# Performance work log

Hardware: AMD Instinct MI355X
Metric: run time of the kernel (lower is better)

## Reference

```python
import jax, jax.numpy as jnp
import numpy as np

B, C, HH, WW, HEADS = 4, 64, 256, 256, 8
CH = C // HEADS              # 8 per-head dim
HID = int(C * 2.66)          # 170
EPS_LN = 1e-5
EPS = 1e-6
QK_NORM = 1.0
# crpe windows for 8 heads: {3:2, 5:3, 7:3}; each conv input split = head_split*Ch*2
WINDOWS = [(3, 2), (5, 3), (7, 3)]


def conv2d(x, w, b=None, groups=1, pad=0):
    out = jax.lax.conv_general_dilated(
        x, w, (1, 1), [(pad, pad), (pad, pad)],
        dimension_numbers=('NCHW', 'OIHW', 'NCHW'), feature_group_count=groups)
    return out if b is None else out + b[None, :, None, None]


def setup_inputs() -> dict:
    key = jax.random.key(0)
    ks = jax.random.split(key, 32)
    p = lambda k, shp, s=0.05: jax.random.normal(k, shp, jnp.float32) * s
    inp = {
        'x': jax.random.normal(ks[0], (B, HH * WW, C), jnp.float32),
        'ln1_w': jnp.ones((C,), jnp.float32) + p(ks[1], (C,), 0.01),
        'sca_w': p(ks[2], (C, C, 1, 1)), 'sca_b': p(ks[3], (C,)),
        'dw1_w': p(ks[4], (2 * C, C, 1, 1)),          # 1x1 dim->2dim
        'dw2_w': p(ks[5], (C, 2, 3, 3)),              # grouped 3x3, groups=C, in/grp=2
        'qkv_w': p(ks[6], (3 * C, C, 1, 1)),
        'qkv_dw_w': p(ks[7], (3 * C, 1, 3, 3)),       # depthwise 3x3
        'temperature': jnp.ones((HEADS, 1, 1), jnp.float32),
        'r3_w': p(ks[8], (2, 2 * CH, 3, 3)), 'r3_b': p(ks[9], (2,)),
        'r5_w': p(ks[10], (3, 2 * CH, 5, 5)), 'r5_b': p(ks[11], (3,)),
        'r7_w': p(ks[12], (3, 2 * CH, 7, 7)), 'r7_b': p(ks[13], (3,)),
        'proj_w': p(ks[14], (C, C, 1, 1)),
        'ln2_w': jnp.ones((C,), jnp.float32) + p(ks[15], (C,), 0.01),
        'pin_w': p(ks[16], (2 * HID, C, 1, 1)),
        'ffn_dw_w': p(ks[17], (2 * HID, 1, 3, 3)),
        'pout_w': p(ks[18], (C, HID, 1, 1)),
        'H': HH, 'W': WW,
    }
    return inp


def biasfree_ln(x, w):
    # BiasFree LayerNorm over channel dim of NCHW (var only, no mean-subtract)
    sigma = jnp.var(x, axis=1, keepdims=True)
    return x / jnp.sqrt(sigma + EPS_LN) * w[None, :, None, None]


def refine_att(q, k, H, W, convs):
    # q: (B,h,N,Ch)  k: (B,h,Ch,N) -> per-head conv relative position map (B,h,N,1)
    b, h, N, Ch = q.shape
    q_img = q.transpose(0, 1, 3, 2).reshape(b, h, Ch, H, W)
    k_img = k.reshape(b, h, Ch, H, W)
    qk = jnp.concatenate([q_img, k_img], axis=2).reshape(b, h * 2 * Ch, H, W)
    splits = np.cumsum([s * 2 * Ch for _, s in WINDOWS])[:-1]
    parts = jnp.split(qk, splits, axis=1)
    outs = [conv2d(xp, wt, bs, groups=g, pad=win // 2)
            for (win, g), (wt, bs), xp in zip(WINDOWS, convs, parts)]
    att = jnp.concatenate(outs, axis=1)           # (b, h, H, W)
    return att.reshape(b, h, 1, H * W).transpose(0, 1, 3, 2)  # (b,h,N,1)


def attention(x, sca_w, sca_b, dw1_w, dw2_w, qkv_w, qkv_dw_w, temperature,
              refine_convs, proj_w, H, W):
    b, c, _, _ = x.shape
    N = H * W
    xsca = conv2d(jnp.mean(x, axis=(2, 3), keepdims=True), sca_w, sca_b)
    x1 = conv2d(conv2d(x, dw1_w), dw2_w, groups=c, pad=1)
    qkv = conv2d(conv2d(x, qkv_w), qkv_dw_w, groups=3 * c, pad=1)
    q, k, v = jnp.split(qkv, 3, axis=1)
    q = q.reshape(b, HEADS, CH, N).transpose(0, 1, 3, 2)  # b h N Ch
    k = k.reshape(b, HEADS, CH, N)                        # b h Ch N
    v = v.reshape(b, HEADS, CH, N).transpose(0, 1, 3, 2)  # b h N Ch
    q = q / (jnp.linalg.norm(q, axis=-1, keepdims=True) / QK_NORM + EPS)
    k = k / (jnp.linalg.norm(k, axis=-2, keepdims=True) / QK_NORM + EPS)
    refine_w = jax.nn.sigmoid(refine_att(q, k, H, W, refine_convs))
    attn = k @ v                                           # b h Ch Ch
    out_num = jnp.sum(v, axis=-2, keepdims=True) + q @ attn
    ksum = jnp.sum(k, axis=-1, keepdims=True)              # b h Ch 1
    out_den = jnp.asarray(N, q.dtype) + q @ ksum + EPS     # b h N 1 (bcast to Ch)
    out = out_num / out_den * temperature
    out = out * refine_w
    out = out.transpose(0, 1, 3, 2).reshape(b, c, H, W)
    out = out * xsca * jax.nn.gelu(x1, approximate=False)
    return conv2d(out, proj_w)


def feedforward(x, pin_w, ffn_dw_w, pout_w):
    h = conv2d(x, pin_w)
    h = conv2d(h, ffn_dw_w, groups=2 * HID, pad=1)
    h1, h2 = jnp.split(h, 2, axis=1)
    return conv2d(jax.nn.gelu(h1, approximate=False) * h2, pout_w)


def reference(x, ln1_w, sca_w, sca_b, dw1_w, dw2_w, qkv_w, qkv_dw_w, temperature,
              r3_w, r3_b, r5_w, r5_b, r7_w, r7_b, proj_w, ln2_w,
              pin_w, ffn_dw_w, pout_w, H, W):
    b = x.shape[0]
    xi = x.reshape(b, H, W, C).transpose(0, 3, 1, 2)  # NCHW
    refine_convs = [(r3_w, r3_b), (r5_w, r5_b), (r7_w, r7_b)]
    xi = xi + attention(biasfree_ln(xi, ln1_w), sca_w, sca_b, dw1_w, dw2_w,
                        qkv_w, qkv_dw_w, temperature, refine_convs, proj_w, H, W)
    xi = xi + feedforward(biasfree_ln(xi, ln2_w), pin_w, ffn_dw_w, pout_w)
    return xi
```

## Files before the change

### kernel.cpp

```cpp
#include <hip/hip_runtime.h>
#include <math.h>
#include <stdio.h>

#define BB 4
#define NP 65536

typedef unsigned short u16;
typedef unsigned int u32;
typedef __attribute__((ext_vector_type(8))) short short8;
typedef __attribute__((ext_vector_type(4))) float f32x4;

__device__ __forceinline__ float bf2f(u16 u) { return __uint_as_float((u32)u << 16); }
__device__ __forceinline__ u16 f2bf(float f) {
  u32 u = __float_as_uint(f);
  u = (u + 0x7FFFu + ((u >> 16) & 1u)) >> 16;
  return (u16)u;
}
__device__ __forceinline__ float gelu_f(float x) {
  return 0.5f * x * (1.f + erff(x * 0.70710678118654752f));
}

__global__ __launch_bounds__(256) void k_trans_stats(const float* __restrict__ x,
                                                     float* __restrict__ xi,
                                                     u16* __restrict__ xb1,
                                                     float* __restrict__ meanraw) {
  __shared__ float tile[64 * 65];
  __shared__ float s1a[64], s2a[64], sig[64], cm[64];
  int b = blockIdx.y;
  long n0 = (long)blockIdx.x * 64;
  int t = threadIdx.x;
  for (int i = t; i < 4096; i += 256) {
    int nl = i >> 6, c = i & 63;
    tile[nl * 65 + c] = x[((long)b * NP + n0 + nl) * 64 + c];
  }
  if (t < 64) { s1a[t] = 0.f; s2a[t] = 0.f; cm[t] = 0.f; }
  __syncthreads();
  {
    int nl = t & 63, part = t >> 6;
    float p1 = 0.f, p2 = 0.f;
    for (int cc = 0; cc < 16; cc++) {
      float v = tile[nl * 65 + part * 16 + cc];
      p1 += v; p2 += v * v;
    }
    atomicAdd(&s1a[nl], p1); atomicAdd(&s2a[nl], p2);
  }
  __syncthreads();
  if (t < 64) {
    float m = s1a[t] * (1.f / 64.f);
    float var = s2a[t] * (1.f / 64.f) - m * m;
    sig[t] = rsqrtf(var + 1e-5f);
  }
  __syncthreads();
  int nl = t & 63;
  int part = t >> 6;
  float sgv = sig[nl];
  for (int j = 0; j < 16; j++) {
    int i = t + 256 * j;
    int c = i >> 6;
    float v = tile[nl * 65 + c];
    xi[((long)b * 64 + c) * NP + n0 + nl] = v;
    float a = v * sgv;
    for (int off = 32; off; off >>= 1) a += __shfl_down(a, off);
    if ((t & 63) == 0) atomicAdd(&cm[c], a);
  }
  {
    u16* rp = xb1 + ((long)b * NP + n0 + nl) * 64 + part * 16;
    uint4 pk[2];
    u32 tmp[8];
#pragma unroll
    for (int g = 0; g < 2; g++) {
#pragma unroll
      for (int e = 0; e < 4; e++) {
        float v0 = tile[nl * 65 + part * 16 + g * 8 + 2 * e] * sgv;
        float v1 = tile[nl * 65 + part * 16 + g * 8 + 2 * e + 1] * sgv;
        tmp[e] = (u32)f2bf(v0) | ((u32)f2bf(v1) << 16);
      }
      pk[g].x = tmp[0]; pk[g].y = tmp[1]; pk[g].z = tmp[2]; pk[g].w = tmp[3];
      *(uint4*)(rp + g * 8) = pk[g];
    }
  }
  __syncthreads();
  if (t < 64) atomicAdd(&meanraw[b * 64 + t], cm[t]);
}

__global__ void k_xsca(const float* __restrict__ meanraw, const float* __restrict__ lnw,
                       const float* __restrict__ sca_w, const float* __restrict__ sca_b,
                       float* __restrict__ xsca) {
  int t = threadIdx.x;
  int b = t >> 6, co = t & 63;
  float a = sca_b[co];
  for (int ci = 0; ci < 64; ci++)
    a += sca_w[co * 64 + ci] * meanraw[b * 64 + ci] * lnw[ci] * (1.f / 65536.f);
  xsca[t] = a;
}

__global__ void k_foldW1b(const float* __restrict__ qkv_w, const float* __restrict__ dw1_w,
                          const float* __restrict__ lnw, u16* __restrict__ W1b) {
  int i = blockIdx.x * 256 + threadIdx.x;
  if (i < 320 * 64) {
    int co = i >> 6, ci = i & 63;
    float w = (co < 192) ? qkv_w[co * 64 + ci] : dw1_w[(co - 192) * 64 + ci];
    W1b[i] = f2bf(w * lnw[ci]);
  }
}
__global__ void k_foldW2b(const float* __restrict__ pin_w, const float* __restrict__ lnw,
                          u16* __restrict__ W2b) {
  int i = blockIdx.x * 256 + threadIdx.x;
  if (i < 384 * 64) {
    int co = i >> 6, ci = i & 63;
    float v = 0.f;
    if (co < 340) {
      int pair = co >> 1, which = co & 1;
      v = pin_w[(pair + which * 170) * 64 + ci] * lnw[ci];
    }
    W2b[i] = f2bf(v);
  }
}
__global__ void k_foldWpb(const float* __restrict__ w, u16* __restrict__ Wpb) {
  int i = blockIdx.x * 256 + threadIdx.x;
  if (i < 4096) Wpb[i] = f2bf(w[i]);
}
__global__ void k_tpoutb(const float* __restrict__ w, u16* __restrict__ Wob) {
  int i = blockIdx.x * 256 + threadIdx.x;
  if (i < 64 * 192) {
    int co = i / 192, ci = i - co * 192;
    Wob[i] = (ci < 170) ? f2bf(w[co * 170 + ci]) : (u16)0;
  }
}

template <int EPI>
__global__ __launch_bounds__(256) void k_mgemm(const u16* __restrict__ in, long in_bs,
                                               const u16* __restrict__ W,
                                               u16* __restrict__ outp, long out_bs,
                                               float* __restrict__ xo,
                                               u16* __restrict__ xb2r) {
  int t = threadIdx.x;
  int lane = t & 63, wv = t >> 6;
  int l15 = lane & 15, quad = lane >> 4;
  int pxw = blockIdx.x * 256 + wv * 64;
  int co0 = blockIdx.y * 64;
  int b = blockIdx.z;
  const u16* inb = in + (long)b * in_bs;

  short8 aw[4][2];
#pragma unroll
  for (int t4 = 0; t4 < 4; t4++)
#pragma unroll
    for (int kf = 0; kf < 2; kf++)
      aw[t4][kf] = *(const short8*)(W + (long)(co0 + t4 * 16 + l15) * 64 + kf * 32 + quad * 8);

  f32x4 acc[4][4];
#pragma unroll
  for (int t4 = 0; t4 < 4; t4++)
#pragma unroll
    for (int p = 0; p < 4; p++) acc[t4][p] = (f32x4){0.f, 0.f, 0.f, 0.f};

#pragma unroll
  for (int p = 0; p < 4; p++) {
    long px = pxw + p * 16 + l15;
    short8 bf0 = *(const short8*)(inb + px * 64 + quad * 8);
    short8 bf1 = *(const short8*)(inb + px * 64 + 32 + quad * 8);
#pragma unroll
    for (int t4 = 0; t4 < 4; t4++) {
      acc[t4][p] = __builtin_amdgcn_mfma_f32_16x16x32_bf16(aw[t4][0], bf0, acc[t4][p], 0, 0, 0);
      acc[t4][p] = __builtin_amdgcn_mfma_f32_16x16x32_bf16(aw[t4][1], bf1, acc[t4][p], 0, 0, 0);
    }
  }

  if (EPI == 0) {
    u16* ob = outp + (long)b * out_bs;
#pragma unroll
    for (int t4 = 0; t4 < 4; t4++)
#pragma unroll
      for (int p = 0; p < 4; p++) {
#pragma unroll
        for (int reg = 0; reg < 4; reg++) {
          int co = co0 + t4 * 16 + quad * 4 + reg;
          ob[(long)co * NP + pxw + p * 16 + l15] = f2bf(acc[t4][p][reg]);
        }
      }
  } else {
#pragma unroll
    for (int p = 0; p < 4; p++) {
      long px = pxw + p * 16 + l15;
      float xv[16];
      float s1 = 0.f, s2 = 0.f;
#pragma unroll
      for (int t4 = 0; t4 < 4; t4++)
#pragma unroll
        for (int reg = 0; reg < 4; reg++) {
          int co = t4 * 16 + quad * 4 + reg;
          float v = xo[((long)b * 64 + co) * NP + px] + acc[t4][p][reg];
          xv[t4 * 4 + reg] = v;
          s1 += v; s2 += v * v;
        }
      s1 += __shfl_xor(s1, 16); s2 += __shfl_xor(s2, 16);
      s1 += __shfl_xor(s1, 32); s2 += __shfl_xor(s2, 32);
      float m = s1 * (1.f / 64.f);
      float var = s2 * (1.f / 64.f) - m * m;
      float sg = rsqrtf(var + 1e-5f);
#pragma unroll
      for (int t4 = 0; t4 < 4; t4++)
#pragma unroll
        for (int reg = 0; reg < 4; reg++) {
          int co = t4 * 16 + quad * 4 + reg;
          xo[((long)b * 64 + co) * NP + px] = xv[t4 * 4 + reg];
        }
      u16* rp = xb2r + ((long)b * NP + px) * 64;
#pragma unroll
      for (int t4 = 0; t4 < 4; t4++) {
        u32 u0 = (u32)f2bf(xv[t4 * 4 + 0] * sg) | ((u32)f2bf(xv[t4 * 4 + 1] * sg) << 16);
        u32 u1 = (u32)f2bf(xv[t4 * 4 + 2] * sg) | ((u32)f2bf(xv[t4 * 4 + 3] * sg) << 16);
        uint2 pk; pk.x = u0; pk.y = u1;
        *(uint2*)(rp + t4 * 16 + quad * 4) = pk;
      }
    }
  }
}

__device__ __forceinline__ void dw4(const u16* __restrict__ img, int y, int x0, int lane,
                                    const float* __restrict__ w9, float d[4]) {
  d[0] = 0.f; d[1] = 0.f; d[2] = 0.f; d[3] = 0.f;
#pragma unroll
  for (int dy = -1; dy <= 1; dy++) {
    int r = y + dy;
    float v1, v2, v3, v4;
    if ((unsigned)r < 256u) {
      ushort4 u = *(const ushort4*)(img + r * 256 + x0);
      v1 = bf2f(u.x); v2 = bf2f(u.y); v3 = bf2f(u.z); v4 = bf2f(u.w);
    } else { v1 = 0.f; v2 = 0.f; v3 = 0.f; v4 = 0.f; }
    float v0 = __shfl_up(v4, 1);  if (lane == 0)  v0 = 0.f;
    float v5 = __shfl_down(v1, 1); if (lane == 63) v5 = 0.f;
    float w0 = w9[(dy + 1) * 3], w1 = w9[(dy + 1) * 3 + 1], w2 = w9[(dy + 1) * 3 + 2];
    d[0] += w0 * v0 + w1 * v1 + w2 * v2;
    d[1] += w0 * v1 + w1 * v2 + w2 * v3;
    d[2] += w0 * v2 + w1 * v3 + w2 * v4;
    d[3] += w0 * v3 + w1 * v4 + w2 * v5;
  }
}

__global__ __launch_bounds__(256) void k_dwqkv(const u16* __restrict__ P,
                                               const float* __restrict__ dww,
                                               u16* __restrict__ Qn, u16* __restrict__ Kn,
                                               u16* __restrict__ Vn) {
  int t = threadIdx.x;
  int lane = t & 63, wv = t >> 6;
  int by = blockIdx.y;
  int ph = by >> 3, h = by & 7;
  int b = blockIdx.z;
  int y = blockIdx.x * 4 + wv;
  int x0 = lane * 4;
  long n = (long)y * 256 + x0;
  int cbase = ph * 64 + h * 8;
  const u16* Pb = P + ((long)b * 192 + cbase) * NP;
  const float* wb = dww + cbase * 9;

  float v[8][4];
#pragma unroll
  for (int c = 0; c < 8; c++)
    dw4(Pb + (long)c * NP, y, x0, lane, wb + c * 9, v[c]);

  if (ph < 2) {
    float s2[4] = {0.f, 0.f, 0.f, 0.f};
#pragma unroll
    for (int c = 0; c < 8; c++)
#pragma unroll
      for (int j = 0; j < 4; j++) s2[j] += v[c][j] * v[c][j];
#pragma unroll
    for (int j = 0; j < 4; j++) s2[j] = 1.f / (sqrtf(s2[j]) + 1e-6f);
#pragma unroll
    for (int c = 0; c < 8; c++)
#pragma unroll
      for (int j = 0; j < 4; j++) v[c][j] *= s2[j];
  }
  u16* dst = (ph == 0) ? Qn : (ph == 1) ? Kn : Vn;
#pragma unroll
  for (int c = 0; c < 8; c++) {
    ushort4 st;
    st.x = f2bf(v[c][0]); st.y = f2bf(v[c][1]);
    st.z = f2bf(v[c][2]); st.w = f2bf(v[c][3]);
    *(ushort4*)(dst + ((long)b * 64 + h * 8 + c) * NP + n) = st;
  }
}

__global__ __launch_bounds__(256) void k_stats(const u16* __restrict__ Kn,
                                               const u16* __restrict__ Vn,
                                               float* __restrict__ stats) {
  int t = threadIdx.x;
  int lane = t & 63;
  int h = blockIdx.y, b = blockIdx.z;
  long px = (long)blockIdx.x * 1024 + t * 4;
  const u16* Kb = Kn + ((long)b * 64 + h * 8) * NP + px;
  const u16* Vb = Vn + ((long)b * 64 + h * 8) * NP + px;
  float kf[8][4], vf[8][4];
#pragma unroll
  for (int c = 0; c < 8; c++) {
    ushort4 ku = *(const ushort4*)(Kb + (long)c * NP);
    kf[c][0] = bf2f(ku.x); kf[c][1] = bf2f(ku.y);
    kf[c][2] = bf2f(ku.z); kf[c][3] = bf2f(ku.w);
  }
#pragma unroll
  for (int c = 0; c < 8; c++) {
    ushort4 vu = *(const ushort4*)(Vb + (long)c * NP);
    vf[c][0] = bf2f(vu.x); vf[c][1] = bf2f(vu.y);
    vf[c][2] = bf2f(vu.z); vf[c][3] = bf2f(vu.w);
  }
  __shared__ float sred[80];
  if (t < 80) sred[t] = 0.f;
  __syncthreads();
#pragma unroll
  for (int i = 0; i < 8; i++) {
#pragma unroll
    for (int j = 0; j < 8; j++) {
      float a = kf[i][0] * vf[j][0] + kf[i][1] * vf[j][1] +
                kf[i][2] * vf[j][2] + kf[i][3] * vf[j][3];
      a += __shfl_xor(a, 1); a += __shfl_xor(a, 2); a += __shfl_xor(a, 4);
      a += __shfl_xor(a, 8); a += __shfl_xor(a, 16); a += __shfl_xor(a, 32);
      if (lane == ((i * 8 + j) & 63)) atomicAdd(&sred[i * 8 + j], a);
    }
    {
      float a = kf[i][0] + kf[i][1] + kf[i][2] + kf[i][3];
      a += __shfl_xor(a, 1); a += __shfl_xor(a, 2); a += __shfl_xor(a, 4);
      a += __shfl_xor(a, 8); a += __shfl_xor(a, 16); a += __shfl_xor(a, 32);
      if (lane == ((64 + i) & 63)) atomicAdd(&sred[64 + i], a);
    }
    {
      float a = vf[i][0] + vf[i][1] + vf[i][2] + vf[i][3];
      a += __shfl_xor(a, 1); a += __shfl_xor(a, 2); a += __shfl_xor(a, 4);
      a += __shfl_xor(a, 8); a += __shfl_xor(a, 16); a += __shfl_xor(a, 32);
      if (lane == ((72 + i) & 63)) atomicAdd(&sred[72 + i], a);
    }
  }
  __syncthreads();
  if (t < 80) atomicAdd(&stats[((long)b * 8 + h) * 80 + t], sred[t]);
}

__global__ __launch_bounds__(256) void k_dwg(const u16* __restrict__ P,
                                             const float* __restrict__ dw2_w,
                                             u16* __restrict__ G) {
  int t = threadIdx.x;
  int lane = t & 63, wv = t >> 6;
  int c = blockIdx.y, b = blockIdx.z;
  int y = blockIdx.x * 4 + wv;
  int x0 = lane * 4;
  long n = (long)y * 256 + x0;
  const u16* Pb = P + (long)b * 128 * NP;
  float d1[4], d2[4];
  dw4(Pb + (long)(2 * c) * NP, y, x0, lane, dw2_w + c * 18, d1);
  dw4(Pb + (long)(2 * c + 1) * NP, y, x0, lane, dw2_w + c * 18 + 9, d2);
  ushort4 st;
  st.x = f2bf(gelu_f(d1[0] + d2[0])); st.y = f2bf(gelu_f(d1[1] + d2[1]));
  st.z = f2bf(gelu_f(d1[2] + d2[2])); st.w = f2bf(gelu_f(d1[3] + d2[3]));
  *(ushort4*)(G + ((long)b * 64 + c) * NP + n) = st;
}

__global__ __launch_bounds__(256) void k_dwgate(const u16* __restrict__ P,
                                                const float* __restrict__ dww,
                                                u16* __restrict__ Hb) {
  int t = threadIdx.x;
  int lane = t & 63, wv = t >> 6;
  int c = blockIdx.y, b = blockIdx.z;
  int y = blockIdx.x * 4 + wv;
  int x0 = lane * 4;
  long n = (long)y * 256 + x0;
  const u16* Pb = P + (long)b * 384 * NP;
  float d1[4], d2[4];
  dw4(Pb + (long)(2 * c) * NP, y, x0, lane, dww + c * 9, d1);
  dw4(Pb + (long)(2 * c + 1) * NP, y, x0, lane, dww + (170 + c) * 9, d2);
  ushort4 st;
  st.x = f2bf(gelu_f(d1[0]) * d2[0]); st.y = f2bf(gelu_f(d1[1]) * d2[1]);
  st.z = f2bf(gelu_f(d1[2]) * d2[2]); st.w = f2bf(gelu_f(d1[3]) * d2[3]);
  *(ushort4*)(Hb + ((long)b * 170 + c) * NP + n) = st;
}

__device__ __forceinline__ float bfe_elem(uint2 v, int e) {
  u32 w = (e < 2) ? v.x : v.y;
  return bf2f((e & 1) ? (u16)(w >> 16) : (u16)w);
}

template <int WIN>
__device__ __forceinline__ void dwacc(const u16* __restrict__ img, int y, int x0, int lane,
                                      const float* __restrict__ w, float a[4]) {
  const int R = WIN / 2;
#pragma unroll
  for (int dy = -R; dy <= R; dy++) {
    int r = y + dy;
    uint2 q; q.x = 0u; q.y = 0u;
    if ((unsigned)r < 256u) q = *(const uint2*)(img + r * 256 + x0);
    uint2 ql, qr;
    ql.x = (u32)__shfl_up((int)q.x, 1);  ql.y = (u32)__shfl_up((int)q.y, 1);
    qr.x = (u32)__shfl_down((int)q.x, 1); qr.y = (u32)__shfl_down((int)q.y, 1);
    if (lane == 0)  { ql.x = 0u; ql.y = 0u; }
    if (lane == 63) { qr.x = 0u; qr.y = 0u; }
    float f[4 + 2 * R];
#pragma unroll
    for (int i = 0; i < R; i++) f[i] = bfe_elem(ql, 4 - R + i);
    f[R + 0] = bf2f((u16)q.x); f[R + 1] = bf2f((u16)(q.x >> 16));
    f[R + 2] = bf2f((u16)q.y); f[R + 3] = bf2f((u16)(q.y >> 16));
#pragma unroll
    for (int i = 0; i < R; i++) f[R + 4 + i] = bfe_elem(qr, i);
    const float* wr = w + (dy + R) * WIN;
#pragma unroll
    for (int dx = 0; dx < WIN; dx++) {
      float wv = wr[dx];
      a[0] += wv * f[dx];     a[1] += wv * f[dx + 1];
      a[2] += wv * f[dx + 2]; a[3] += wv * f[dx + 3];
    }
  }
}

template <int WIN>
__device__ void refine_body(const u16* __restrict__ Qh, const u16* __restrict__ Kh,
                            const float* __restrict__ wp, float bias,
                            float* __restrict__ ro, int y, int x0, int lane) {
  float a[4] = {bias, bias, bias, bias};
#pragma unroll
  for (int ph = 0; ph < 2; ph++) {
    const u16* src = ph ? Kh : Qh;
#pragma unroll 2
    for (int ch = 0; ch < 8; ch++)
      dwacc<WIN>(src + (long)ch * NP, y, x0, lane, wp + (ph * 8 + ch) * WIN * WIN, a);
  }
  float4 o;
  o.x = 1.f / (1.f + expf(-a[0])); o.y = 1.f / (1.f + expf(-a[1]));
  o.z = 1.f / (1.f + expf(-a[2])); o.w = 1.f / (1.f + expf(-a[3]));
  *(float4*)(ro + (long)y * 256 + x0) = o;
}

__global__ __launch_bounds__(256) void k_refine(
    const u16* __restrict__ Qn, const u16* __restrict__ Kn,
    const float* __restrict__ r3w, const float* __restrict__ r3b,
    const float* __restrict__ r5w, const float* __restrict__ r5b,
    const float* __restrict__ r7w, const float* __restrict__ r7b,
    float* __restrict__ refW) {
  int t = threadIdx.x, lane = t & 63, wv = t >> 6;
  int h = (blockIdx.y + 5) & 7;
  int b = blockIdx.z;
  int y = blockIdx.x * 4 + wv, x0 = lane * 4;
  const u16* Qh = Qn + ((long)b * 64 + h * 8) * NP;
  const u16* Kh = Kn + ((long)b * 64 + h * 8) * NP;
  float* ro = refW + ((long)(b * 8 + h)) * NP;
  if (h < 2)      refine_body<3>(Qh, Kh, r3w + h * 16 * 9, r3b[h], ro, y, x0, lane);
  else if (h < 5) refine_body<5>(Qh, Kh, r5w + (h - 2) * 16 * 25, r5b[h - 2], ro, y, x0, lane);
  else            refine_body<7>(Qh, Kh, r7w + (h - 5) * 16 * 49, r7b[h - 5], ro, y, x0, lane);
}

__global__ __launch_bounds__(256) void k_attn(
    const u16* __restrict__ Qn, const float* __restrict__ stats,
    const float* __restrict__ refw, const float* __restrict__ temp,
    const float* __restrict__ xsca, const u16* __restrict__ G,
    u16* __restrict__ Orows) {
  int b = blockIdx.y;
  int t = threadIdx.x;
  __shared__ float s[640];
  __shared__ float sx[64];
  for (int i = t; i < 640; i += 256) s[i] = stats[(long)b * 640 + i];
  if (t < 64) sx[t] = xsca[b * 64 + t];
  __syncthreads();
  long n = (long)blockIdx.x * 256 + t;
  u16* rp = Orows + ((long)b * NP + n) * 64;
#pragma unroll
  for (int h = 0; h < 8; h++) {
    const float* sh = s + h * 80;
    float q[8];
#pragma unroll
    for (int i = 0; i < 8; i++) q[i] = bf2f(Qn[((long)b * 64 + h * 8 + i) * NP + n]);
    float den = 65536.f + 1e-6f;
#pragma unroll
    for (int i = 0; i < 8; i++) den += q[i] * sh[64 + i];
    float tr = temp[h] * refw[((long)b * 8 + h) * NP + n] / den;
    u32 pk[4];
#pragma unroll
    for (int j2 = 0; j2 < 4; j2++) {
      float o01[2];
#pragma unroll
      for (int e = 0; e < 2; e++) {
        int j = j2 * 2 + e;
        float num = sh[72 + j];
#pragma unroll
        for (int i = 0; i < 8; i++) num += q[i] * sh[i * 8 + j];
        int ci = h * 8 + j;
        o01[e] = num * tr * sx[ci] * bf2f(G[((long)b * 64 + ci) * NP + n]);
      }
      pk[j2] = (u32)f2bf(o01[0]) | ((u32)f2bf(o01[1]) << 16);
    }
    uint4 v; v.x = pk[0]; v.y = pk[1]; v.z = pk[2]; v.w = pk[3];
    *(uint4*)(rp + h * 8) = v;
  }
}

__global__ __launch_bounds__(256) void k_pout(const u16* __restrict__ Hb,
                                              const u16* __restrict__ Wob,
                                              float* __restrict__ xo) {
  __shared__ u16 tile[64 * 196];
  int t = threadIdx.x;
  int lane = t & 63, wv = t >> 6;
  int l15 = lane & 15, quad = lane >> 4;
  int b = blockIdx.z;
  int px0 = blockIdx.x * 64;
  const u16* ib = Hb + (long)b * 170 * NP + px0;
#pragma unroll
  for (int i = 0; i < 12; i++) {
    int task = t + i * 256;
    int q = task >> 6, px = task & 63;
    int ci0 = q * 4;
    u32 w0 = 0u, w1 = 0u;
    if (ci0 < 170)     w0 = (u32)ib[(long)ci0 * NP + px];
    if (ci0 + 1 < 170) w0 |= ((u32)ib[(long)(ci0 + 1) * NP + px]) << 16;
    if (ci0 + 2 < 170) w1 = (u32)ib[(long)(ci0 + 2) * NP + px];
    if (ci0 + 3 < 170) w1 |= ((u32)ib[(long)(ci0 + 3) * NP + px]) << 16;
    uint2 pk; pk.x = w0; pk.y = w1;
    *(uint2*)(tile + px * 196 + ci0) = pk;
  }
  __syncthreads();

  f32x4 acc[4];
#pragma unroll
  for (int t4 = 0; t4 < 4; t4++) acc[t4] = (f32x4){0.f, 0.f, 0.f, 0.f};
  const u16* tb = tile + (wv * 16 + l15) * 196;
#pragma unroll
  for (int kf = 0; kf < 6; kf++) {
    union { uint2 u2[2]; short8 s8; } cv;
    cv.u2[0] = *(const uint2*)(tb + kf * 32 + quad * 8);
    cv.u2[1] = *(const uint2*)(tb + kf * 32 + quad * 8 + 4);
    short8 bfr = cv.s8;
#pragma unroll
    for (int t4 = 0; t4 < 4; t4++) {
      short8 aw = *(const short8*)(Wob + (long)(t4 * 16 + l15) * 192 + kf * 32 + quad * 8);
      acc[t4] = __builtin_amdgcn_mfma_f32_16x16x32_bf16(aw, bfr, acc[t4], 0, 0, 0);
    }
  }
  long pxg = px0 + wv * 16 + l15;
  float* xb = xo + (long)b * 64 * NP;
#pragma unroll
  for (int t4 = 0; t4 < 4; t4++)
#pragma unroll
    for (int reg = 0; reg < 4; reg++) {
      int co = t4 * 16 + quad * 4 + reg;
      xb[(long)co * NP + pxg] += acc[t4][reg];
    }
}

extern "C" void kernel_launch(void* const* d_in, const int* in_sizes, int n_in,
                              void* d_out, int out_size, void* d_ws, size_t ws_size,
                              hipStream_t stream) {
  const float* x        = (const float*)d_in[0];
  const float* ln1_w    = (const float*)d_in[1];
  const float* sca_w    = (const float*)d_in[2];
  const float* sca_b    = (const float*)d_in[3];
  const float* dw1_w    = (const float*)d_in[4];
  const float* dw2_w    = (const float*)d_in[5];
  const float* qkv_w    = (const float*)d_in[6];
  const float* qkv_dw_w = (const float*)d_in[7];
  const float* temp     = (const float*)d_in[8];
  const float* r3w = (const float*)d_in[9],  *r3b = (const float*)d_in[10];
  const float* r5w = (const float*)d_in[11], *r5b = (const float*)d_in[12];
  const float* r7w = (const float*)d_in[13], *r7b = (const float*)d_in[14];
  const float* proj_w   = (const float*)d_in[15];
  const float* ln2_w    = (const float*)d_in[16];
  const float* pin_w    = (const float*)d_in[17];
  const float* ffn_dw_w = (const float*)d_in[18];
  const float* pout_w   = (const float*)d_in[19];
  float* out = (float*)d_out;
  char* wsb = (char*)d_ws;

  const size_t Mi = 1048576;
  u16* xb1   = (u16*)(wsb);
  u16* Qn    = (u16*)(wsb + 32 * Mi);
  u16* Kn    = (u16*)(wsb + 64 * Mi);
  u16* G     = (u16*)(wsb + 96 * Mi);
  u16* Preg  = (u16*)(wsb + 128 * Mi);
  float* refW    = (float*)(wsb + 224 * Mi);
  float* Fm      = (float*)(wsb + 232 * Mi);
  float* stats   = Fm;
  float* meanraw = Fm + 2560;
  float* xscab   = Fm + 2816;
  u16* Wob       = (u16*)(Fm + 3072);
  u16* W1b = (u16*)(Fm + 13952);
  u16* W2b = W1b + 20480;
  u16* Wpb = W2b + 24576;
  u16* xb2 = xb1;
  u16* Orows = Kn;
  u16* Hb = Qn;
  u16* Vn = G;

  const size_t needed = 232 * Mi + 13952 * 4 + (20480 + 24576 + 4096) * 2;
  if (ws_size < needed) {
    fprintf(stderr, "kernel_launch: ws_size %zu < needed %zu\n", ws_size, needed);
    return;
  }

  hipMemsetAsync(stats, 0, (2560 + 256) * 4, stream);
  k_foldW1b<<<80, 256, 0, stream>>>(qkv_w, dw1_w, ln1_w, W1b);
  k_foldW2b<<<96, 256, 0, stream>>>(pin_w, ln2_w, W2b);
  k_foldWpb<<<16, 256, 0, stream>>>(proj_w, Wpb);
  k_tpoutb<<<48, 256, 0, stream>>>(pout_w, Wob);

  k_trans_stats<<<dim3(1024, BB), 256, 0, stream>>>(x, out, xb1, meanraw);
  k_xsca<<<1, 256, 0, stream>>>(meanraw, ln1_w, sca_w, sca_b, xscab);

  k_mgemm<0><<<dim3(256, 3, BB), 256, 0, stream>>>(xb1, (long)NP * 64, W1b,
                                                   Preg, 192L * NP, nullptr, nullptr);
  k_dwqkv<<<dim3(64, 24, BB), 256, 0, stream>>>(Preg, qkv_dw_w, Qn, Kn, Vn);
  k_stats<<<dim3(64, 8, BB), 256, 0, stream>>>(Kn, Vn, stats);

  k_mgemm<0><<<dim3(256, 2, BB), 256, 0, stream>>>(xb1, (long)NP * 64, W1b + 192 * 64,
                                                   Preg, 128L * NP, nullptr, nullptr);
  k_dwg<<<dim3(64, 64, BB), 256, 0, stream>>>(Preg, dw2_w, G);

  k_refine<<<dim3(64, 8, BB), 256, 0, stream>>>(Qn, Kn, r3w, r3b, r5w, r5b, r7w, r7b, refW);
  k_attn<<<dim3(256, BB), 256, 0, stream>>>(Qn, stats, refW, temp, xscab, G, Orows);

  k_mgemm<1><<<dim3(256, 1, BB), 256, 0, stream>>>(Orows, (long)NP * 64, Wpb,
                                                   nullptr, 0, out, xb2);

  for (int pass = 0; pass < 2; pass++) {
    k_mgemm<0><<<dim3(256, 6, 2), 256, 0, stream>>>(xb2 + (long)pass * 2 * NP * 64,
                                                    (long)NP * 64, W2b,
                                                    Preg, 384L * NP, nullptr, nullptr);
    k_dwgate<<<dim3(64, 170, 2), 256, 0, stream>>>(Preg, ffn_dw_w,
                                                   Hb + (long)pass * 2 * 170 * NP);
  }
  k_pout<<<dim3(1024, 1, BB), 256, 0, stream>>>(Hb, Wob, out);
}
```

Before: 854.9 us.

## Compute two output rows per wave in refine conv with packed float2 FMAs

The refine relative-position conv kernel now has each wave produce two adjacent output rows, so every loaded input row feeds both outputs and row loads drop by nearly half. Accumulation uses float2 vectors so the compiler can emit packed FMA instructions. Only the shuffles a given window needs are issued, and bf16 unpacking is done with cheaper bit ops. The grid is flattened so that the 8 heads, which have different window sizes, are interleaved within each block to balance load. The channel loop is no longer unrolled and each thread holds more accumulators, which may reduce instruction-level parallelism or raise register pressure.

```diff
diff --git a/kernel.cpp b/kernel.cpp
--- a/kernel.cpp
+++ b/kernel.cpp
@@ -9,6 +9,7 @@
 typedef unsigned int u32;
 typedef __attribute__((ext_vector_type(8))) short short8;
 typedef __attribute__((ext_vector_type(4))) float f32x4;
+typedef __attribute__((ext_vector_type(2))) float f32x2;
 
 __device__ __forceinline__ float bf2f(u16 u) { return __uint_as_float((u32)u << 16); }
 __device__ __forceinline__ u16 f2bf(float f) {
@@ -373,58 +374,79 @@
   *(ushort4*)(Hb + ((long)b * 170 + c) * NP + n) = st;
 }
 
-__device__ __forceinline__ float bfe_elem(uint2 v, int e) {
-  u32 w = (e < 2) ? v.x : v.y;
-  return bf2f((e & 1) ? (u16)(w >> 16) : (u16)w);
-}
+__device__ __forceinline__ float wlo(u32 w) { return __uint_as_float(w << 16); }
+__device__ __forceinline__ float whi(u32 w) { return __uint_as_float(w & 0xFFFF0000u); }
 
 template <int WIN>
-__device__ __forceinline__ void dwacc(const u16* __restrict__ img, int y, int x0, int lane,
-                                      const float* __restrict__ w, float a[4]) {
+__device__ void refine2(const u16* __restrict__ Qh, const u16* __restrict__ Kh,
+                        const float* __restrict__ wp, float bias,
+                        float* __restrict__ ro, int y0, int x0, int lane) {
   const int R = WIN / 2;
-#pragma unroll
-  for (int dy = -R; dy <= R; dy++) {
-    int r = y + dy;
-    uint2 q; q.x = 0u; q.y = 0u;
-    if ((unsigned)r < 256u) q = *(const uint2*)(img + r * 256 + x0);
-    uint2 ql, qr;
-    ql.x = (u32)__shfl_up((int)q.x, 1);  ql.y = (u32)__shfl_up((int)q.y, 1);
-    qr.x = (u32)__shfl_down((int)q.x, 1); qr.y = (u32)__shfl_down((int)q.y, 1);
-    if (lane == 0)  { ql.x = 0u; ql.y = 0u; }
-    if (lane == 63) { qr.x = 0u; qr.y = 0u; }
-    float f[4 + 2 * R];
-#pragma unroll
-    for (int i = 0; i < R; i++) f[i] = bfe_elem(ql, 4 - R + i);
-    f[R + 0] = bf2f((u16)q.x); f[R + 1] = bf2f((u16)(q.x >> 16));
-    f[R + 2] = bf2f((u16)q.y); f[R + 3] = bf2f((u16)(q.y >> 16));
-#pragma unroll
-    for (int i = 0; i < R; i++) f[R + 4 + i] = bfe_elem(qr, i);
-    const float* wr = w + (dy + R) * WIN;
-#pragma unroll
-    for (int dx = 0; dx < WIN; dx++) {
-      float wv = wr[dx];
-      a[0] += wv * f[dx];     a[1] += wv * f[dx + 1];
-      a[2] += wv * f[dx + 2]; a[3] += wv * f[dx + 3];
-    }
-  }
-}
-
-template <int WIN>
-__device__ void refine_body(const u16* __restrict__ Qh, const u16* __restrict__ Kh,
-                            const float* __restrict__ wp, float bias,
-                            float* __restrict__ ro, int y, int x0, int lane) {
-  float a[4] = {bias, bias, bias, bias};
+  f32x2 a0a = {bias, bias}, a0b = {bias, bias};
+  f32x2 a1a = {0.f, 0.f}, a1b = {0.f, 0.f};
 #pragma unroll
   for (int ph = 0; ph < 2; ph++) {
     const u16* src = ph ? Kh : Qh;
-#pragma unroll 2
-    for (int ch = 0; ch < 8; ch++)
-      dwacc<WIN>(src + (long)ch * NP, y, x0, lane, wp + (ph * 8 + ch) * WIN * WIN, a);
-  }
-  float4 o;
-  o.x = 1.f / (1.f + expf(-a[0])); o.y = 1.f / (1.f + expf(-a[1]));
-  o.z = 1.f / (1.f + expf(-a[2])); o.w = 1.f / (1.f + expf(-a[3]));
-  *(float4*)(ro + (long)y * 256 + x0) = o;
+#pragma unroll 1
+    for (int ch = 0; ch < 8; ch++) {
+      const u16* img = src + (long)ch * NP;
+      const float* wc = wp + (ph * 8 + ch) * WIN * WIN;
+#pragma unroll
+      for (int r = -R; r <= 1 + R; r++) {
+        int row = y0 + r;
+        uint2 q; q.x = 0u; q.y = 0u;
+        if ((unsigned)row < 256u) q = *(const uint2*)(img + row * 256 + x0);
+        float f[4 + 2 * R];
+        f[R + 0] = wlo(q.x); f[R + 1] = whi(q.x);
+        f[R + 2] = wlo(q.y); f[R + 3] = whi(q.y);
+        {
+          u32 qly = (u32)__shfl_up((int)q.y, 1);
+          u32 qrx = (u32)__shfl_down((int)q.x, 1);
+          if (lane == 0)  qly = 0u;
+          if (lane == 63) qrx = 0u;
+          f[R - 1] = whi(qly); f[R + 4] = wlo(qrx);
+          if (R >= 2) { f[R - 2] = wlo(qly); f[R + 5] = whi(qrx); }
+          if (R >= 3) {
+            u32 qlx = (u32)__shfl_up((int)q.x, 1);
+            u32 qry = (u32)__shfl_down((int)q.y, 1);
+            if (lane == 0)  qlx = 0u;
+            if (lane == 63) qry = 0u;
+            f[0] = whi(qlx); f[R + 6] = wlo(qry);
+          }
+        }
+        f32x2 fp[3 + 2 * R];
+#pragma unroll
+        for (int i = 0; i < 3 + 2 * R; i++) fp[i] = (f32x2){f[i], f[i + 1]};
+        if (r <= R) {
+          const float* w0 = wc + (r + R) * WIN;
+#pragma unroll
+          for (int dx = 0; dx < WIN; dx++) {
+            float wv = w0[dx];
+            f32x2 w2 = {wv, wv};
+            a0a += w2 * fp[dx];
+            a0b += w2 * fp[dx + 2];
+          }
+        }
+        if (r >= 1 - R) {
+          const float* w1 = wc + (r - 1 + R) * WIN;
+#pragma unroll
+          for (int dx = 0; dx < WIN; dx++) {
+            float wv = w1[dx];
+            f32x2 w2 = {wv, wv};
+            a1a += w2 * fp[dx];
+            a1b += w2 * fp[dx + 2];
+          }
+        }
+      }
+    }
+  }
+  float4 o0, o1;
+  o0.x = 1.f / (1.f + expf(-a0a.x)); o0.y = 1.f / (1.f + expf(-a0a.y));
+  o0.z = 1.f / (1.f + expf(-a0b.x)); o0.w = 1.f / (1.f + expf(-a0b.y));
+  o1.x = 1.f / (1.f + expf(-(a1a.x + bias))); o1.y = 1.f / (1.f + expf(-(a1a.y + bias)));
+  o1.z = 1.f / (1.f + expf(-(a1b.x + bias))); o1.w = 1.f / (1.f + expf(-(a1b.y + bias)));
+  *(float4*)(ro + (long)y0 * 256 + x0) = o0;
+  *(float4*)(ro + (long)(y0 + 1) * 256 + x0) = o1;
 }
 
 __global__ __launch_bounds__(256) void k_refine(
@@ -434,15 +456,18 @@
     const float* __restrict__ r7w, const float* __restrict__ r7b,
     float* __restrict__ refW) {
   int t = threadIdx.x, lane = t & 63, wv = t >> 6;
-  int h = (blockIdx.y + 5) & 7;
-  int b = blockIdx.z;
-  int y = blockIdx.x * 4 + wv, x0 = lane * 4;
+  int u = blockIdx.x * 4 + wv;
+  int h = u & 7;
+  int rest = u >> 3;
+  int b = rest >> 7;
+  int y0 = (rest & 127) * 2;
+  int x0 = lane * 4;
   const u16* Qh = Qn + ((long)b * 64 + h * 8) * NP;
   const u16* Kh = Kn + ((long)b * 64 + h * 8) * NP;
   float* ro = refW + ((long)(b * 8 + h)) * NP;
-  if (h < 2)      refine_body<3>(Qh, Kh, r3w + h * 16 * 9, r3b[h], ro, y, x0, lane);
-  else if (h < 5) refine_body<5>(Qh, Kh, r5w + (h - 2) * 16 * 25, r5b[h - 2], ro, y, x0, lane);
-  else            refine_body<7>(Qh, Kh, r7w + (h - 5) * 16 * 49, r7b[h - 5], ro, y, x0, lane);
+  if (h < 2)      refine2<3>(Qh, Kh, r3w + h * 16 * 9, r3b[h], ro, y0, x0, lane);
+  else if (h < 5) refine2<5>(Qh, Kh, r5w + (h - 2) * 16 * 25, r5b[h - 2], ro, y0, x0, lane);
+  else            refine2<7>(Qh, Kh, r7w + (h - 5) * 16 * 49, r7b[h - 5], ro, y0, x0, lane);
 }
 
 __global__ __launch_bounds__(256) void k_attn(
@@ -608,7 +633,7 @@
                                                    Preg, 128L * NP, nullptr, nullptr);
   k_dwg<<<dim3(64, 64, BB), 256, 0, stream>>>(Preg, dw2_w, G);
 
-  k_refine<<<dim3(64, 8, BB), 256, 0, stream>>>(Qn, Kn, r3w, r3b, r5w, r5b, r7w, r7b, refW);
+  k_refine<<<dim3(1024), 256, 0, stream>>>(Qn, Kn, r3w, r3b, r5w, r5b, r7w, r7b, refW);
   k_attn<<<dim3(256, BB), 256, 0, stream>>>(Qn, stats, refW, temp, xscab, G, Orows);
 
   k_mgemm<1><<<dim3(256, 1, BB), 256, 0, stream>>>(Orows, (long)NP * 64, Wpb,
```

Measured after the change: 844.8 us. No clear change (-1.2%).
